# Optimization experiments

Hardware: AMD Instinct MI355X
Metric: run time of the kernel (lower is better)

## Reference

```python
import jax, jax.numpy as jnp
import numpy as np

N, E = 20000, 100000
IN_CH, HID_CH, EDGE_DIM, NUM_CLASSES = 32, 32, 16, 10


def setup_inputs() -> dict:
    key = jax.random.key(0)
    ks = jax.random.split(key, 20)
    s = 0.05
    inp = {
        "x": jax.random.normal(ks[0], (N, IN_CH), jnp.float32),
        "edge_index": jax.random.randint(ks[1], (2, E), 0, N, jnp.int64),
        "edge_attr": jax.random.normal(ks[2], (E, EDGE_DIM), jnp.float32),
        # edge MLP 1: edge_dim -> in*hid -> in*hid (weights stored as (in, out))
        "e1_w1": jax.random.normal(ks[3], (EDGE_DIM, IN_CH * HID_CH), jnp.float32) * s,
        "e1_b1": jnp.zeros((IN_CH * HID_CH,), jnp.float32),
        "e1_w2": jax.random.normal(ks[4], (IN_CH * HID_CH, IN_CH * HID_CH), jnp.float32) * s,
        "e1_b2": jnp.zeros((IN_CH * HID_CH,), jnp.float32),
        "root1": jax.random.normal(ks[5], (IN_CH, HID_CH), jnp.float32) * s,
        "bias1": jnp.zeros((HID_CH,), jnp.float32),
        # edge MLP 2: edge_dim -> hid*hid -> hid*hid
        "e2_w1": jax.random.normal(ks[6], (EDGE_DIM, HID_CH * HID_CH), jnp.float32) * s,
        "e2_b1": jnp.zeros((HID_CH * HID_CH,), jnp.float32),
        "e2_w2": jax.random.normal(ks[7], (HID_CH * HID_CH, HID_CH * HID_CH), jnp.float32) * s,
        "e2_b2": jnp.zeros((HID_CH * HID_CH,), jnp.float32),
        "root2": jax.random.normal(ks[8], (HID_CH, HID_CH), jnp.float32) * s,
        "bias2": jnp.zeros((HID_CH,), jnp.float32),
        "lin_w": jax.random.normal(ks[9], (HID_CH, NUM_CLASSES), jnp.float32) * s,
        "lin_b": jnp.zeros((NUM_CLASSES,), jnp.float32),
    }
    return inp


def _nnconv_mean(x, src, dst, edge_attr, w1, b1, w2, b2, root, bias, in_ch, out_ch, n_nodes):
    # edge MLP -> per-edge weight matrix [E, in_ch, out_ch]
    h = jax.nn.relu(edge_attr @ w1 + b1) @ w2 + b2
    W = h.reshape(-1, in_ch, out_ch)
    # message: x_j @ W_e (gather source features, per-edge matmul)
    msg = jnp.einsum('ei,eio->eo', x[src], W)
    # scatter-mean to target nodes
    agg = jax.ops.segment_sum(msg, dst, num_segments=n_nodes)
    cnt = jax.ops.segment_sum(jnp.ones((msg.shape[0],), msg.dtype), dst, num_segments=n_nodes)
    mean = agg / jnp.maximum(cnt, 1.0)[:, None]
    return mean + x @ root + bias


def reference(x, edge_index, edge_attr,
              e1_w1, e1_b1, e1_w2, e1_b2, root1, bias1,
              e2_w1, e2_b1, e2_w2, e2_b2, root2, bias2,
              lin_w, lin_b):
    src, dst = edge_index[0], edge_index[1]
    n = x.shape[0]
    h = jax.nn.relu(_nnconv_mean(x, src, dst, edge_attr, e1_w1, e1_b1, e1_w2, e1_b2,
                                 root1, bias1, IN_CH, HID_CH, n))
    # dropout p=0.5 is identity in eval mode
    h = jax.nn.relu(_nnconv_mean(h, src, dst, edge_attr, e2_w1, e2_b1, e2_w2, e2_b2,
                                 root2, bias2, HID_CH, HID_CH, n))
    return h @ lin_w + lin_b
```

## Files before the change

### kernel.cpp

```cpp
#include <hip/hip_runtime.h>

typedef __attribute__((ext_vector_type(8))) short sh8;
typedef __attribute__((ext_vector_type(4))) float f32x4;

#define E_EDGES 100000
#define E_PAD   100096
#define N_NODES 20000

#define BAR() do { __builtin_amdgcn_sched_barrier(0); __builtin_amdgcn_s_barrier(); __builtin_amdgcn_sched_barrier(0); } while (0)

__device__ __forceinline__ unsigned short f2bf(float f) {
  union { float f; unsigned int u; } v; v.f = f;
  unsigned int r = v.u + 0x7FFFu + ((v.u >> 16) & 1u);
  return (unsigned short)(r >> 16);
}

__device__ __forceinline__ void async16(const void* g, void* l) {
  __builtin_amdgcn_global_load_lds((const __attribute__((address_space(1))) unsigned int*)g,
                                   (__attribute__((address_space(3))) unsigned int*)l,
                                   16, 0, 0);
}

__global__ void transpose_w2_kernel(const float* __restrict__ w2, unsigned short* __restrict__ w2t) {
  __shared__ float tile[32][33];
  int b = blockIdx.x;
  int bx = b & 31, by = b >> 5;
  int lx = threadIdx.x & 31, ly = threadIdx.x >> 5;
#pragma unroll
  for (int j = 0; j < 4; ++j)
    tile[ly + j*8][lx] = w2[(size_t)(by*32 + ly + j*8)*1024 + bx*32 + lx];
  __syncthreads();
#pragma unroll
  for (int j = 0; j < 4; ++j)
    w2t[(size_t)(bx*32 + ly + j*8)*1024 + by*32 + lx] = f2bf(tile[lx][ly + j*8]);
}

__global__ __launch_bounds__(256)
void edge_mlp1_kernel(const float* __restrict__ ea, const float* __restrict__ w1,
                      const float* __restrict__ b1, unsigned short* __restrict__ h1) {
  __shared__ float eas[16][16];
  const int tid = threadIdx.x;
  const int e0 = blockIdx.x * 16;
  {
    int g = tid >> 4, d = tid & 15;
    int ge = e0 + g;
    eas[g][d] = (ge < E_EDGES) ? ea[(size_t)ge*16 + d] : 0.f;
  }
  __syncthreads();
  const int c0 = tid * 4;
  float4 bb = *(const float4*)(b1 + c0);
  float4 acc[16];
#pragma unroll
  for (int g = 0; g < 16; ++g) acc[g] = bb;
#pragma unroll
  for (int d = 0; d < 16; ++d) {
    float4 w = *(const float4*)(w1 + (size_t)d*1024 + c0);
#pragma unroll
    for (int g = 0; g < 16; ++g) {
      float ev = eas[g][d];
      acc[g].x += ev*w.x; acc[g].y += ev*w.y; acc[g].z += ev*w.z; acc[g].w += ev*w.w;
    }
  }
#pragma unroll
  for (int g = 0; g < 16; ++g) {
    ushort4 o;
    if (e0 + g < E_EDGES) {
      o.x = f2bf(fmaxf(acc[g].x, 0.f)); o.y = f2bf(fmaxf(acc[g].y, 0.f));
      o.z = f2bf(fmaxf(acc[g].z, 0.f)); o.w = f2bf(fmaxf(acc[g].w, 0.f));
    } else {
      o.x = o.y = o.z = o.w = 0;
    }
    *(ushort4*)(h1 + (size_t)(e0 + g)*1024 + c0) = o;
  }
}

__global__ void count_kernel(const int* __restrict__ dst, float* __restrict__ cnt) {
  int t = blockIdx.x*256 + threadIdx.x;
  if (t < E_EDGES) atomicAdd(&cnt[dst[t]], 1.0f);
}

__global__ __launch_bounds__(512, 1)
void gemm_scatter_kernel(const unsigned short* __restrict__ h1,
                         const unsigned short* __restrict__ w2t,
                         const float* __restrict__ b2,
                         const float* __restrict__ xin,
                         const int* __restrict__ src,
                         const int* __restrict__ dst,
                         float* __restrict__ agg) {
  __shared__ __align__(16) unsigned char lds[163840];
  float* msgA = (float*)lds;
  float* msgB = (float*)(lds + 33792);
  float (*xg)[8] = (float (*)[8])(lds + 67584);
  int* dsts = (int*)(lds + 75776);

  const int tid  = threadIdx.x;
  const int wave = tid >> 6, lane = tid & 63;
  const int wm = wave >> 2, wn = wave & 3;
  const int lr = lane >> 4, lc = lane & 15;

  const int bid = blockIdx.x;
  const int xcd = bid & 7, idx = bid >> 3;
  const int logical = (xcd < 4 ? xcd*196 : 784 + (xcd - 4)*195) + idx;
  const int tile_m = logical >> 2, tile_n = logical & 3;
  const long e0 = (long)tile_m * 256, n0 = (long)tile_n * 256;

  const unsigned short* Ag = h1  + (size_t)e0*1024;
  const unsigned short* Bg = w2t + (size_t)n0*1024;

  const int l8   = lane >> 3;
  const int scol = 8*((lane & 7) ^ l8);
  const int srow = wave*8 + l8;
  const int swzb = (lc & 7) << 4;

#define ABUF(i) (lds + (i)*32768)
#define BBUF(i) (lds + 98304 + (i)*32768)
#define STAGE_A(bi, kt) do { _Pragma("unroll")                                      \
    for (int j = 0; j < 4; ++j)                                                     \
      async16(Ag + (size_t)(srow + 64*j)*1024 + (kt)*64 + scol,                     \
              ABUF(bi) + (wave*8 + 64*j)*128); } while (0)
#define STAGE_B(bi, kt) do { _Pragma("unroll")                                      \
    for (int j = 0; j < 4; ++j)                                                     \
      async16(Bg + (size_t)(srow + 64*j)*1024 + (kt)*64 + scol,                     \
              BBUF(bi) + (wave*8 + 64*j)*128); } while (0)

  f32x4 acc[8][4];
#pragma unroll
  for (int m = 0; m < 8; ++m)
#pragma unroll
    for (int n = 0; n < 4; ++n) acc[m][n] = (f32x4){0.f, 0.f, 0.f, 0.f};

  STAGE_B(0, 0);
  STAGE_A(0, 0);
  STAGE_A(1, 1);

#pragma unroll
  for (int kt = 0; kt < 16; ++kt) {
    if (kt == 15) asm volatile("s_waitcnt vmcnt(0)" ::: "memory");
    else          asm volatile("s_waitcnt vmcnt(4)" ::: "memory");
    BAR();
    if (kt + 1 < 16) STAGE_B((kt + 1) & 1, kt + 1);
    if (kt + 2 < 16) STAGE_A((kt + 2) % 3, kt + 2);
    const char* Ab = (const char*)ABUF(kt % 3);
    const char* Bb = (const char*)BBUF(kt & 1);
#pragma unroll
    for (int kk = 0; kk < 2; ++kk) {
      sh8 a[8], b[4];
#pragma unroll
      for (int n = 0; n < 4; ++n)
        b[n] = *(const sh8*)(Bb + (wn*64 + n*16 + lc)*128 + ((kk*64 + lr*16) ^ swzb));
#pragma unroll
      for (int m = 0; m < 8; ++m)
        a[m] = *(const sh8*)(Ab + (wm*128 + m*16 + lc)*128 + ((kk*64 + lr*16) ^ swzb));
      __builtin_amdgcn_s_setprio(1);
#pragma unroll
      for (int m = 0; m < 8; ++m)
#pragma unroll
        for (int n = 0; n < 4; ++n)
          acc[m][n] = __builtin_amdgcn_mfma_f32_16x16x32_bf16(a[m], b[n], acc[m][n], 0, 0, 0);
      __builtin_amdgcn_s_setprio(0);
    }
  }
#undef STAGE_A
#undef STAGE_B
#undef ABUF
#undef BBUF

  __syncthreads();
  {
    int e = tid >> 1, half = tid & 1;
    long ge = e0 + e;
    float4 v = make_float4(0.f, 0.f, 0.f, 0.f);
    if (ge < E_EDGES) v = *(const float4*)(xin + (size_t)src[ge]*32 + tile_n*8 + half*4);
    *(float4*)&xg[e][half*4] = v;
    if (tid < 256) dsts[tid] = (e0 + tid < E_EDGES) ? dst[e0 + tid] : -1;
  }
  float b2c[4];
#pragma unroll
  for (int n = 0; n < 4; ++n) b2c[n] = b2[n0 + wn*64 + n*16 + lc];
  __syncthreads();

  if ((wn & 1) == 0) {
    float* mb = (wn == 0) ? msgA : msgB;
#pragma unroll
    for (int m = 0; m < 8; ++m)
#pragma unroll
      for (int r = 0; r < 4; ++r) {
        int e = wm*128 + m*16 + lr*4 + r;
        float x0 = xg[e][2*wn], x1 = xg[e][2*wn + 1];
        mb[e*33 + lc]      = (acc[m][0][r] + b2c[0])*x0 + (acc[m][2][r] + b2c[2])*x1;
        mb[e*33 + lc + 16] = (acc[m][1][r] + b2c[1])*x0 + (acc[m][3][r] + b2c[3])*x1;
      }
  }
  __syncthreads();
  if ((wn & 1) == 1) {
    float* mb = (wn == 1) ? msgA : msgB;
#pragma unroll
    for (int m = 0; m < 8; ++m)
#pragma unroll
      for (int r = 0; r < 4; ++r) {
        int e = wm*128 + m*16 + lr*4 + r;
        float x0 = xg[e][2*wn], x1 = xg[e][2*wn + 1];
        mb[e*33 + lc]      += (acc[m][0][r] + b2c[0])*x0 + (acc[m][2][r] + b2c[2])*x1;
        mb[e*33 + lc + 16] += (acc[m][1][r] + b2c[1])*x0 + (acc[m][3][r] + b2c[3])*x1;
      }
  }
  __syncthreads();
  for (int t = tid; t < 256*32; t += 512) {
    int e = t >> 5, o = t & 31;
    int dn = dsts[e];
    if (dn >= 0) atomicAdd(&agg[(size_t)dn*32 + o], msgA[e*33 + o] + msgB[e*33 + o]);
  }
}

__global__ void node_update_kernel(const float* __restrict__ agg, const float* __restrict__ cnt,
                                   const float* __restrict__ xin, const float* __restrict__ root,
                                   const float* __restrict__ bias, float* __restrict__ outp) {
  int t = blockIdx.x*256 + threadIdx.x;
  if (t >= N_NODES*32) return;
  int n = t >> 5, i = t & 31;
  const float* xr = xin + (size_t)n*32;
  float s = bias[i];
#pragma unroll
  for (int j = 0; j < 32; ++j) s += xr[j]*root[j*32 + i];
  float c = cnt[n]; c = c > 1.f ? c : 1.f;
  float v = agg[t]/c + s;
  outp[t] = fmaxf(v, 0.f);
}

__global__ void final_linear_kernel(const float* __restrict__ h, const float* __restrict__ lw,
                                    const float* __restrict__ lb, float* __restrict__ out) {
  int t = blockIdx.x*256 + threadIdx.x;
  if (t >= N_NODES*10) return;
  int n = t / 10, k = t % 10;
  const float* hr = h + (size_t)n*32;
  float s = lb[k];
#pragma unroll
  for (int i = 0; i < 32; ++i) s += hr[i]*lw[i*10 + k];
  out[t] = s;
}

extern "C" void kernel_launch(void* const* d_in, const int* in_sizes, int n_in,
                              void* d_out, int out_size, void* d_ws, size_t ws_size,
                              hipStream_t stream) {
  const float* x     = (const float*)d_in[0];
  const int*   ei    = (const int*)d_in[1];
  const float* ea    = (const float*)d_in[2];
  const float* e1w1  = (const float*)d_in[3];
  const float* e1b1  = (const float*)d_in[4];
  const float* e1w2  = (const float*)d_in[5];
  const float* e1b2  = (const float*)d_in[6];
  const float* root1 = (const float*)d_in[7];
  const float* bias1 = (const float*)d_in[8];
  const float* e2w1  = (const float*)d_in[9];
  const float* e2b1  = (const float*)d_in[10];
  const float* e2w2  = (const float*)d_in[11];
  const float* e2b2  = (const float*)d_in[12];
  const float* root2 = (const float*)d_in[13];
  const float* bias2 = (const float*)d_in[14];
  const float* linw  = (const float*)d_in[15];
  const float* linb  = (const float*)d_in[16];
  const int* srcp = ei;
  const int* dstp = ei + E_EDGES;

  char* ws = (char*)d_ws;
  size_t off = 0;
  auto alloc = [&](size_t bytes) { void* p = ws + off; off += (bytes + 255) & ~(size_t)255; return p; };
  unsigned short* h1buf = (unsigned short*)alloc((size_t)E_PAD*1024*2);
  unsigned short* w2t   = (unsigned short*)alloc((size_t)1024*1024*2);
  float* agg  = (float*)alloc((size_t)N_NODES*32*4);
  float* cnt  = (float*)alloc((size_t)N_NODES*4);
  float* out1 = (float*)alloc((size_t)N_NODES*32*4);
  float* hbuf = (float*)alloc((size_t)N_NODES*32*4);
  (void)ws_size; (void)n_in; (void)in_sizes; (void)out_size;

  hipMemsetAsync(agg, 0, (size_t)N_NODES*32*4, stream);
  hipMemsetAsync(cnt, 0, (size_t)N_NODES*4, stream);
  count_kernel<<<(E_EDGES + 255)/256, 256, 0, stream>>>(dstp, cnt);

  const int gemm_grid = (E_PAD/256) * 4;

  transpose_w2_kernel<<<1024, 256, 0, stream>>>(e1w2, w2t);
  edge_mlp1_kernel<<<E_PAD/16, 256, 0, stream>>>(ea, e1w1, e1b1, h1buf);
  gemm_scatter_kernel<<<gemm_grid, 512, 0, stream>>>(h1buf, w2t, e1b2, x, srcp, dstp, agg);
  node_update_kernel<<<(N_NODES*32 + 255)/256, 256, 0, stream>>>(agg, cnt, x, root1, bias1, out1);

  hipMemsetAsync(agg, 0, (size_t)N_NODES*32*4, stream);
  transpose_w2_kernel<<<1024, 256, 0, stream>>>(e2w2, w2t);
  edge_mlp1_kernel<<<E_PAD/16, 256, 0, stream>>>(ea, e2w1, e2b1, h1buf);
  gemm_scatter_kernel<<<gemm_grid, 512, 0, stream>>>(h1buf, w2t, e2b2, out1, srcp, dstp, agg);
  node_update_kernel<<<(N_NODES*32 + 255)/256, 256, 0, stream>>>(agg, cnt, out1, root2, bias2, hbuf);

  final_linear_kernel<<<(N_NODES*10 + 255)/256, 256, 0, stream>>>(hbuf, linw, linb, (float*)d_out);
}
```

Baseline: 727.2 us.

## Load pre-blocked W2 fragments directly from global into registers, shrink LDS

The transpose kernel now writes W2 in an MFMA-fragment-blocked bf16 layout, so each wave loads its B operands straight from global/L2 into registers instead of staging B through LDS. LDS drops to three A buffers, and the A staging loads are interleaved with the MFMA groups while the next k-step's B fragments are prefetched into registers. This removes B's LDS traffic and footprint but puts global-load latency for B on the critical path and depends on L2 hit rates for W2.

```diff
diff --git a/kernel.cpp b/kernel.cpp
--- a/kernel.cpp
+++ b/kernel.cpp
@@ -21,7 +21,7 @@
                                    16, 0, 0);
 }
 
-__global__ void transpose_w2_kernel(const float* __restrict__ w2, unsigned short* __restrict__ w2t) {
+__global__ void transpose_w2_kernel(const float* __restrict__ w2, unsigned short* __restrict__ w2b) {
   __shared__ float tile[32][33];
   int b = blockIdx.x;
   int bx = b & 31, by = b >> 5;
@@ -31,8 +31,12 @@
     tile[ly + j*8][lx] = w2[(size_t)(by*32 + ly + j*8)*1024 + bx*32 + lx];
   __syncthreads();
 #pragma unroll
-  for (int j = 0; j < 4; ++j)
-    w2t[(size_t)(bx*32 + ly + j*8)*1024 + by*32 + lx] = f2bf(tile[lx][ly + j*8]);
+  for (int j = 0; j < 4; ++j) {
+    int n = bx*32 + ly + j*8;
+    int k = by*32 + lx;
+    size_t idx = ((size_t)(n >> 4)*128 + (k >> 3))*128 + (n & 15)*8 + (k & 7);
+    w2b[idx] = f2bf(tile[lx][ly + j*8]);
+  }
 }
 
 __global__ __launch_bounds__(256)
@@ -81,13 +85,13 @@
 
 __global__ __launch_bounds__(512, 1)
 void gemm_scatter_kernel(const unsigned short* __restrict__ h1,
-                         const unsigned short* __restrict__ w2t,
+                         const unsigned short* __restrict__ w2b,
                          const float* __restrict__ b2,
                          const float* __restrict__ xin,
                          const int* __restrict__ src,
                          const int* __restrict__ dst,
                          float* __restrict__ agg) {
-  __shared__ __align__(16) unsigned char lds[163840];
+  __shared__ __align__(16) unsigned char lds[98304];
   float* msgA = (float*)lds;
   float* msgB = (float*)(lds + 33792);
   float (*xg)[8] = (float (*)[8])(lds + 67584);
@@ -104,24 +108,16 @@
   const int tile_m = logical >> 2, tile_n = logical & 3;
   const long e0 = (long)tile_m * 256, n0 = (long)tile_n * 256;
 
-  const unsigned short* Ag = h1  + (size_t)e0*1024;
-  const unsigned short* Bg = w2t + (size_t)n0*1024;
-
-  const int l8   = lane >> 3;
-  const int scol = 8*((lane & 7) ^ l8);
-  const int srow = wave*8 + l8;
+  const unsigned short* Ag = h1 + (size_t)e0*1024;
+  const int rj   = lane >> 3;
+  const int scol = 8*((lane & 7) ^ rj);
   const int swzb = (lc & 7) << 4;
 
-#define ABUF(i) (lds + (i)*32768)
-#define BBUF(i) (lds + 98304 + (i)*32768)
-#define STAGE_A(bi, kt) do { _Pragma("unroll")                                      \
-    for (int j = 0; j < 4; ++j)                                                     \
-      async16(Ag + (size_t)(srow + 64*j)*1024 + (kt)*64 + scol,                     \
-              ABUF(bi) + (wave*8 + 64*j)*128); } while (0)
-#define STAGE_B(bi, kt) do { _Pragma("unroll")                                      \
-    for (int j = 0; j < 4; ++j)                                                     \
-      async16(Bg + (size_t)(srow + 64*j)*1024 + (kt)*64 + scol,                     \
-              BBUF(bi) + (wave*8 + 64*j)*128); } while (0)
+  const char* Bb = (const char*)w2b + (size_t)(tile_n*16 + wn*4)*32768 + lr*256 + lc*16;
+
+#define STAGE_Q(dstbase, q, pn) \
+    async16(Ag + (size_t)((q)*64 + wave*8 + rj)*1024 + (size_t)(pn)*64 + scol, \
+            (dstbase) + (q)*8192 + wave*1024)
 
   f32x4 acc[8][4];
 #pragma unroll
@@ -129,42 +125,68 @@
 #pragma unroll
     for (int n = 0; n < 4; ++n) acc[m][n] = (f32x4){0.f, 0.f, 0.f, 0.f};
 
-  STAGE_B(0, 0);
-  STAGE_A(0, 0);
-  STAGE_A(1, 1);
-
-#pragma unroll
+#pragma unroll
+  for (int q = 0; q < 4; ++q) STAGE_Q(lds, q, 0);
+#pragma unroll
+  for (int q = 0; q < 4; ++q) STAGE_Q(lds + 32768, q, 1);
+  sh8 bc[4];
+#pragma unroll
+  for (int n = 0; n < 4; ++n) bc[n] = *(const sh8*)(Bb + n*32768);
+  asm volatile("s_waitcnt vmcnt(8)" ::: "memory");
+  BAR();
+
+  int sr = 0, sw = 2;
   for (int kt = 0; kt < 16; ++kt) {
-    if (kt == 15) asm volatile("s_waitcnt vmcnt(0)" ::: "memory");
-    else          asm volatile("s_waitcnt vmcnt(4)" ::: "memory");
-    BAR();
-    if (kt + 1 < 16) STAGE_B((kt + 1) & 1, kt + 1);
-    if (kt + 2 < 16) STAGE_A((kt + 2) % 3, kt + 2);
-    const char* Ab = (const char*)ABUF(kt % 3);
-    const char* Bb = (const char*)BBUF(kt & 1);
-#pragma unroll
-    for (int kk = 0; kk < 2; ++kk) {
-      sh8 a[8], b[4];
-#pragma unroll
-      for (int n = 0; n < 4; ++n)
-        b[n] = *(const sh8*)(Bb + (wn*64 + n*16 + lc)*128 + ((kk*64 + lr*16) ^ swzb));
-#pragma unroll
-      for (int m = 0; m < 8; ++m)
-        a[m] = *(const sh8*)(Ab + (wm*128 + m*16 + lc)*128 + ((kk*64 + lr*16) ^ swzb));
+    const char* Ab = (const char*)(lds + sr*32768);
+    char* Aw = (char*)(lds + sw*32768);
+    const int pn = (kt + 2 < 16) ? (kt + 2) : 0;
+    const int ktn = (kt + 1) & 15;
+
+    sh8 b1[4];
+#pragma unroll
+    for (int n = 0; n < 4; ++n)
+      b1[n] = *(const sh8*)(Bb + n*32768 + kt*2048 + 1024);
+
+#pragma unroll
+    for (int mp = 0; mp < 4; ++mp) {
+      sh8 a0 = *(const sh8*)(Ab + (wm*128 + (2*mp    )*16 + lc)*128 + ((lr*16) ^ swzb));
+      sh8 a1 = *(const sh8*)(Ab + (wm*128 + (2*mp + 1)*16 + lc)*128 + ((lr*16) ^ swzb));
+      STAGE_Q(Aw, mp, pn);
       __builtin_amdgcn_s_setprio(1);
 #pragma unroll
-      for (int m = 0; m < 8; ++m)
-#pragma unroll
-        for (int n = 0; n < 4; ++n)
-          acc[m][n] = __builtin_amdgcn_mfma_f32_16x16x32_bf16(a[m], b[n], acc[m][n], 0, 0, 0);
+      for (int n = 0; n < 4; ++n) {
+        acc[2*mp  ][n] = __builtin_amdgcn_mfma_f32_16x16x32_bf16(a0, bc[n], acc[2*mp  ][n], 0, 0, 0);
+        acc[2*mp+1][n] = __builtin_amdgcn_mfma_f32_16x16x32_bf16(a1, bc[n], acc[2*mp+1][n], 0, 0, 0);
+      }
       __builtin_amdgcn_s_setprio(0);
     }
-  }
-#undef STAGE_A
-#undef STAGE_B
-#undef ABUF
-#undef BBUF
-
+    __builtin_amdgcn_sched_barrier(0);
+
+#pragma unroll
+    for (int n = 0; n < 4; ++n)
+      bc[n] = *(const sh8*)(Bb + n*32768 + ktn*2048);
+
+#pragma unroll
+    for (int mp = 0; mp < 4; ++mp) {
+      sh8 a0 = *(const sh8*)(Ab + (wm*128 + (2*mp    )*16 + lc)*128 + ((64 + lr*16) ^ swzb));
+      sh8 a1 = *(const sh8*)(Ab + (wm*128 + (2*mp + 1)*16 + lc)*128 + ((64 + lr*16) ^ swzb));
+      __builtin_amdgcn_s_setprio(1);
+#pragma unroll
+      for (int n = 0; n < 4; ++n) {
+        acc[2*mp  ][n] = __builtin_amdgcn_mfma_f32_16x16x32_bf16(a0, b1[n], acc[2*mp  ][n], 0, 0, 0);
+        acc[2*mp+1][n] = __builtin_amdgcn_mfma_f32_16x16x32_bf16(a1, b1[n], acc[2*mp+1][n], 0, 0, 0);
+      }
+      __builtin_amdgcn_s_setprio(0);
+    }
+
+    asm volatile("s_waitcnt vmcnt(8)" ::: "memory");
+    BAR();
+    sr = (sr == 2) ? 0 : sr + 1;
+    sw = (sw == 2) ? 0 : sw + 1;
+  }
+#undef STAGE_Q
+
+  asm volatile("s_waitcnt vmcnt(0)" ::: "memory");
   __syncthreads();
   {
     int e = tid >> 1, half = tid & 1;
@@ -266,7 +288,7 @@
   size_t off = 0;
   auto alloc = [&](size_t bytes) { void* p = ws + off; off += (bytes + 255) & ~(size_t)255; return p; };
   unsigned short* h1buf = (unsigned short*)alloc((size_t)E_PAD*1024*2);
-  unsigned short* w2t   = (unsigned short*)alloc((size_t)1024*1024*2);
+  unsigned short* w2b   = (unsigned short*)alloc((size_t)1024*1024*2);
   float* agg  = (float*)alloc((size_t)N_NODES*32*4);
   float* cnt  = (float*)alloc((size_t)N_NODES*4);
   float* out1 = (float*)alloc((size_t)N_NODES*32*4);
@@ -279,15 +301,15 @@
 
   const int gemm_grid = (E_PAD/256) * 4;
 
-  transpose_w2_kernel<<<1024, 256, 0, stream>>>(e1w2, w2t);
+  transpose_w2_kernel<<<1024, 256, 0, stream>>>(e1w2, w2b);
   edge_mlp1_kernel<<<E_PAD/16, 256, 0, stream>>>(ea, e1w1, e1b1, h1buf);
-  gemm_scatter_kernel<<<gemm_grid, 512, 0, stream>>>(h1buf, w2t, e1b2, x, srcp, dstp, agg);
+  gemm_scatter_kernel<<<gemm_grid, 512, 0, stream>>>(h1buf, w2b, e1b2, x, srcp, dstp, agg);
   node_update_kernel<<<(N_NODES*32 + 255)/256, 256, 0, stream>>>(agg, cnt, x, root1, bias1, out1);
 
   hipMemsetAsync(agg, 0, (size_t)N_NODES*32*4, stream);
-  transpose_w2_kernel<<<1024, 256, 0, stream>>>(e2w2, w2t);
+  transpose_w2_kernel<<<1024, 256, 0, stream>>>(e2w2, w2b);
   edge_mlp1_kernel<<<E_PAD/16, 256, 0, stream>>>(ea, e2w1, e2b1, h1buf);
-  gemm_scatter_kernel<<<gemm_grid, 512, 0, stream>>>(h1buf, w2t, e2b2, out1, srcp, dstp, agg);
+  gemm_scatter_kernel<<<gemm_grid, 512, 0, stream>>>(h1buf, w2b, e2b2, out1, srcp, dstp, agg);
   node_update_kernel<<<(N_NODES*32 + 255)/256, 256, 0, stream>>>(agg, cnt, out1, root2, bias2, hbuf);
 
   final_linear_kernel<<<(N_NODES*10 + 255)/256, 256, 0, stream>>>(hbuf, linw, linb, (float*)d_out);
```

Result: slower. 781.1 us (+7.4%).
